# Performance work log

Hardware: AMD Instinct MI355X
Metric: run time of the kernel (lower is better)

Reference implementation:

```python
import jax, jax.numpy as jnp
import numpy as np

N = 100000
E = 1600000
DIMS = [128, 128, 64]


def _gcn_norm(edge_index, num_nodes):
    # PyG gcn_norm: add self-loops, symmetric normalization D^-1/2 (A+I) D^-1/2
    src, dst = edge_index[0], edge_index[1]
    loop = jnp.arange(num_nodes, dtype=src.dtype)
    src = jnp.concatenate([src, loop])
    dst = jnp.concatenate([dst, loop])
    deg = jax.ops.segment_sum(jnp.ones_like(src, dtype=jnp.float32), dst,
                              num_segments=num_nodes)
    dinv = jnp.where(deg > 0, jax.lax.rsqrt(deg), 0.0)
    w = dinv[src] * dinv[dst]  # [E+N]
    return src, dst, w


def _gcn_conv(x, src, dst, w, W, b):
    # transform first (cheaper when out_dim <= in_dim), then aggregate
    h = x @ W                                   # [N, out]
    msg = h[src] * w[:, None]                   # gather + scale  [E+N, out]
    out = jax.ops.segment_sum(msg, dst, num_segments=x.shape[0])
    return out + b


def setup_inputs() -> dict:
    key = jax.random.key(0)
    ks = jax.random.split(key, 6)
    x = jax.random.normal(ks[0], (N, DIMS[0]), dtype=jnp.float32)
    edge_index = jax.random.randint(ks[1], (2, E), 0, N, dtype=jnp.int64)
    # Glorot-style init for GCNConv weights, zero bias (PyG default)
    W1 = jax.random.normal(ks[2], (DIMS[0], DIMS[1]), dtype=jnp.float32) / np.sqrt(DIMS[0])
    b1 = jnp.zeros((DIMS[1],), dtype=jnp.float32)
    W2 = jax.random.normal(ks[3], (DIMS[1], DIMS[2]), dtype=jnp.float32) / np.sqrt(DIMS[1])
    b2 = jnp.zeros((DIMS[2],), dtype=jnp.float32)
    return {"x": x, "edge_index": edge_index, "W1": W1, "b1": b1, "W2": W2, "b2": b2}


def reference(x, edge_index, W1, b1, W2, b2):
    src, dst, w = _gcn_norm(edge_index, x.shape[0])
    h = _gcn_conv(x, src, dst, w, W1, b1)
    h = jax.nn.relu(h)
    # dropout is identity in eval mode (deterministic reference)
    out = _gcn_conv(h, src, dst, w, W2, b2)
    return out
```

## Files before the change

kernel.cpp:

```cpp
#include <hip/hip_runtime.h>
#include <hip/hip_fp16.h>

#define TPB 256
#define CHUNK 1024
#define EPB 4096
#define CSHIFT 8
#define AGG_BLOCKS 2048

typedef _Float16 half8 __attribute__((ext_vector_type(8)));
typedef float    f32x4 __attribute__((ext_vector_type(4)));


__global__ __launch_bounds__(256) void scanA_kernel(const int* __restrict__ cnt,
                                                    int* __restrict__ row_ptr,
                                                    int* __restrict__ chunk_sums, int n) {
    __shared__ int ls[256];
    const int t    = threadIdx.x;
    const int base = blockIdx.x * CHUNK;
    const int idx  = base + t * 4;
    int4 v = make_int4(0, 0, 0, 0);
    if (idx + 3 < n) v = *(const int4*)(cnt + idx);
    else {
        if (idx + 0 < n) v.x = cnt[idx + 0];
        if (idx + 1 < n) v.y = cnt[idx + 1];
        if (idx + 2 < n) v.z = cnt[idx + 2];
        if (idx + 3 < n) v.w = cnt[idx + 3];
    }
    int s0 = v.x, s1 = s0 + v.y, s2 = s1 + v.z, s3 = s2 + v.w;
    ls[t] = s3;
    __syncthreads();
    for (int off = 1; off < 256; off <<= 1) {
        int xv = (t >= off) ? ls[t - off] : 0;
        __syncthreads();
        ls[t] += xv;
        __syncthreads();
    }
    int excl = (t == 0) ? 0 : ls[t - 1];
    if (idx + 0 < n) row_ptr[idx + 0] = excl;
    if (idx + 1 < n) row_ptr[idx + 1] = excl + s0;
    if (idx + 2 < n) row_ptr[idx + 2] = excl + s1;
    if (idx + 3 < n) row_ptr[idx + 3] = excl + s2;
    if (t == 255) chunk_sums[blockIdx.x] = ls[255];
}

__global__ __launch_bounds__(256) void scanB_kernel(int* __restrict__ chunk_sums, int nch) {
    __shared__ int ls[256];
    const int t = threadIdx.x;
    ls[t] = (t < nch) ? chunk_sums[t] : 0;
    __syncthreads();
    for (int off = 1; off < 256; off <<= 1) {
        int xv = (t >= off) ? ls[t - off] : 0;
        __syncthreads();
        ls[t] += xv;
        __syncthreads();
    }
    if (t < nch) chunk_sums[t] = (t == 0) ? 0 : ls[t - 1];
}


__global__ __launch_bounds__(256) void hist_kernel(const int* __restrict__ dst,
                                                   int* __restrict__ hist_g,
                                                   int e, int nbc, int nblk) {
    __shared__ int hs[512];
    const int t = threadIdx.x;
    for (int i = t; i < nbc; i += 256) hs[i] = 0;
    __syncthreads();
    const int e0  = blockIdx.x * EPB;
    const int lim = min(e0 + EPB, e);
    for (int i = e0 + t; i < lim; i += 256)
        atomicAdd(&hs[dst[i] >> CSHIFT], 1);
    __syncthreads();
    for (int b = t; b < nbc; b += 256)
        hist_g[b * nblk + blockIdx.x] = hs[b];
}

__global__ __launch_bounds__(256) void partition_kernel(const int* __restrict__ src,
                                                        const int* __restrict__ dst,
                                                        const int* __restrict__ hist_scan,
                                                        const int* __restrict__ chunk_sums,
                                                        int* __restrict__ pairs,
                                                        int e, int nbc, int nblk) {
    __shared__ int  hs[512];
    __shared__ int  lscan[512];
    __shared__ int  lfill[512];
    __shared__ int  base_s[512];
    __shared__ int  ls[256];
    __shared__ int2 sp[EPB];
    const int t = threadIdx.x;
    for (int i = t; i < nbc; i += 256) { hs[i] = 0; lfill[i] = 0; }
    __syncthreads();
    const int e0  = blockIdx.x * EPB;
    const int lim = min(e0 + EPB, e);
    for (int i = e0 + t; i < lim; i += 256)
        atomicAdd(&hs[dst[i] >> CSHIFT], 1);
    __syncthreads();
    int v0 = (2 * t     < nbc) ? hs[2 * t]     : 0;
    int v1 = (2 * t + 1 < nbc) ? hs[2 * t + 1] : 0;
    ls[t] = v0 + v1;
    __syncthreads();
    for (int off = 1; off < 256; off <<= 1) {
        int xv = (t >= off) ? ls[t - off] : 0;
        __syncthreads();
        ls[t] += xv;
        __syncthreads();
    }
    int excl = (t == 0) ? 0 : ls[t - 1];
    if (2 * t     < nbc) lscan[2 * t]     = excl;
    if (2 * t + 1 < nbc) lscan[2 * t + 1] = excl + v0;
    for (int b = t; b < nbc; b += 256) {
        int hidx = b * nblk + blockIdx.x;
        base_s[b] = hist_scan[hidx] + chunk_sums[hidx >> 10];
    }
    __syncthreads();
    for (int i = e0 + t; i < lim; i += 256) {
        int d = dst[i];
        int b = d >> CSHIFT;
        int r = atomicAdd(&lfill[b], 1);
        sp[lscan[b] + r] = make_int2(src[i], d);
    }
    __syncthreads();
    const int cnt = lim - e0;
    for (int i = t; i < cnt; i += 256) {
        int2 pr = sp[i];
        int  b  = pr.y >> CSHIFT;
        pairs[base_s[b] + (i - lscan[b])] = pr.x | ((pr.y & 255) << 17);
    }
}

__global__ __launch_bounds__(256) void bucket_finalize_kernel(const int* __restrict__ pairs,
                                                              const int* __restrict__ hist_scan,
                                                              const int* __restrict__ chunk_sums,
                                                              int* __restrict__ row_ptr,
                                                              float* __restrict__ dinv,
                                                              int* __restrict__ csr_src,
                                                              int n, int e, int nbc, int nblk) {
    __shared__ int cnt_s[256];
    __shared__ int fill[256];
    __shared__ int ls[256];
    const int b   = blockIdx.x;
    const int nb0 = b << CSHIFT;
    const int t   = threadIdx.x;
    const int h0  = b * nblk;
    const int r0  = hist_scan[h0] + chunk_sums[h0 >> 10];
    int r1 = e;
    if (b + 1 < nbc) {
        const int h1 = (b + 1) * nblk;
        r1 = hist_scan[h1] + chunk_sums[h1 >> 10];
    }
    cnt_s[t] = 0;
    __syncthreads();
    for (int i = r0 + t; i < r1; i += 256)
        atomicAdd(&cnt_s[pairs[i] >> 17], 1);
    __syncthreads();
    int c = cnt_s[t];
    ls[t] = c;
    __syncthreads();
    for (int off = 1; off < 256; off <<= 1) {
        int xv = (t >= off) ? ls[t - off] : 0;
        __syncthreads();
        ls[t] += xv;
        __syncthreads();
    }
    int excl = (t == 0) ? 0 : ls[t - 1];
    int node = nb0 + t;
    if (node < n) {
        row_ptr[node] = r0 + excl;
        dinv[node]    = rsqrtf((float)(c + 1));
    }
    fill[t] = r0 + excl;
    __syncthreads();
    for (int i = r0 + t; i < r1; i += 256) {
        int pr = pairs[i];
        int p  = atomicAdd(&fill[pr >> 17], 1);
        csr_src[p] = pr & 0x1FFFF;
    }
    if (b == 0 && t == 0) row_ptr[n] = e;
}


__global__ __launch_bounds__(256) void wprep_kernel(const float* __restrict__ W1,
                                                    const float* __restrict__ W2,
                                                    _Float16* __restrict__ wf1g,
                                                    _Float16* __restrict__ wf2g) {
    const int tid = threadIdx.x;
    if (blockIdx.x == 0) {
        for (int f = tid; f < 8 * 4 * 64; f += 256) {
            int c    = f >> 8;
            int i    = (f >> 6) & 3;
            int lane = f & 63;
            int quad = lane >> 4, n = lane & 15;
            const float* wp = W1 + (size_t)(i * 32 + quad * 8) * 128 + c * 16 + n;
            half8 hv;
#pragma unroll
            for (int j = 0; j < 8; ++j) hv[j] = (_Float16)wp[(size_t)j * 128];
            ((half8*)wf1g)[f] = hv;
        }
    } else {
        for (int f = tid; f < 4 * 4 * 64; f += 256) {
            int c    = f >> 8;
            int i    = (f >> 6) & 3;
            int lane = f & 63;
            int quad = lane >> 4, n = lane & 15;
            const float* wp = W2 + (size_t)(i * 32 + quad * 8) * 64 + c * 16 + n;
            half8 hv;
#pragma unroll
            for (int j = 0; j < 8; ++j) hv[j] = (_Float16)wp[(size_t)j * 64];
            ((half8*)wf2g)[f] = hv;
        }
    }
}


template <int M, bool RELU, typename XT>
__global__ __launch_bounds__(256) void gemm_mfma_kernel(const XT* __restrict__ X,
                                                        const _Float16* __restrict__ Wfg,
                                                        const float* __restrict__ dinv,
                                                        __half* __restrict__ H, int nrows) {
    constexpr int NC = M / 16;
    __shared__ __align__(16) _Float16 Wf[NC * 4 * 64 * 8];

    const int tid = threadIdx.x;
    const uint4* wb = (const uint4*)Wfg;
    for (int f = tid; f < NC * 4 * 64; f += 256)
        ((uint4*)Wf)[f] = wb[f];
    __syncthreads();

    const int  wave = tid >> 6, lane = tid & 63;
    const int  quad = lane >> 4, n16 = lane & 15;
    const long rowbase = (long)blockIdx.x * 64 + wave * 16;

    long arow = rowbase + n16;
    const XT* xrow = X + (size_t)(arow < nrows ? arow : 0) * 128;
    half8 a[4];
    if constexpr (sizeof(XT) == 4) {
        const float4* xr = (const float4*)xrow;
#pragma unroll
        for (int i = 0; i < 4; ++i) {
            float4 x0 = xr[i * 8 + quad * 2];
            float4 x1 = xr[i * 8 + quad * 2 + 1];
            if (RELU) {
                x0.x = fmaxf(x0.x, 0.f); x0.y = fmaxf(x0.y, 0.f);
                x0.z = fmaxf(x0.z, 0.f); x0.w = fmaxf(x0.w, 0.f);
                x1.x = fmaxf(x1.x, 0.f); x1.y = fmaxf(x1.y, 0.f);
                x1.z = fmaxf(x1.z, 0.f); x1.w = fmaxf(x1.w, 0.f);
            }
            half8 hv;
            hv[0] = (_Float16)x0.x; hv[1] = (_Float16)x0.y;
            hv[2] = (_Float16)x0.z; hv[3] = (_Float16)x0.w;
            hv[4] = (_Float16)x1.x; hv[5] = (_Float16)x1.y;
            hv[6] = (_Float16)x1.z; hv[7] = (_Float16)x1.w;
            a[i] = hv;
        }
    } else {
        const half8* xr = (const half8*)xrow;
#pragma unroll
        for (int i = 0; i < 4; ++i) {
            half8 hv = xr[i * 4 + quad];
            if (RELU) {
#pragma unroll
                for (int j = 0; j < 8; ++j)
                    hv[j] = (hv[j] > (_Float16)0) ? hv[j] : (_Float16)0;
            }
            a[i] = hv;
        }
    }

    float dv[4];
#pragma unroll
    for (int r = 0; r < 4; ++r) {
        long orow = rowbase + quad * 4 + r;
        dv[r] = (orow < nrows) ? dinv[orow] : 0.f;
    }

    for (int c = 0; c < NC; ++c) {
        f32x4 acc = {0.f, 0.f, 0.f, 0.f};
#pragma unroll
        for (int i = 0; i < 4; ++i) {
            half8 b = ((const half8*)Wf)[(c * 4 + i) * 64 + lane];
            acc = __builtin_amdgcn_mfma_f32_16x16x32_f16(a[i], b, acc, 0, 0, 0);
        }
#pragma unroll
        for (int r = 0; r < 4; ++r) {
            long orow = rowbase + quad * 4 + r;
            if (orow < nrows)
                H[orow * M + c * 16 + n16] = __float2half(acc[r] * dv[r]);
        }
    }
}


__device__ __forceinline__ void add_u4(float2* a, const uint4& u) {
    float2 v0 = __half22float2(*(const __half2*)&u.x);
    float2 v1 = __half22float2(*(const __half2*)&u.y);
    float2 v2 = __half22float2(*(const __half2*)&u.z);
    float2 v3 = __half22float2(*(const __half2*)&u.w);
    a[0].x += v0.x; a[0].y += v0.y;
    a[1].x += v1.x; a[1].y += v1.y;
    a[2].x += v2.x; a[2].y += v2.y;
    a[3].x += v3.x; a[3].y += v3.y;
}


__global__ __launch_bounds__(TPB) void agg_pull128_kernel(const __half* __restrict__ hs,
                                                          const int* __restrict__ csr_src,
                                                          const int* __restrict__ row_ptr,
                                                          const float* __restrict__ dinv,
                                                          const float* __restrict__ bias,
                                                          __half* __restrict__ out, int n) {
    const int wid  = blockIdx.x * (TPB / 64) + (threadIdx.x >> 6);
    const int NW   = gridDim.x * (TPB / 64);
    const int lane = threadIdx.x & 63;
    const int q    = lane >> 4;
    const int sl   = lane & 15;
    if (wid >= n) return;
    const uint4* up   = (const uint4*)hs;
    const uint4* upsl = up + sl;

    const float4* bp = (const float4*)bias;
    const float4 bb0 = bp[2 * sl], bb1 = bp[2 * sl + 1];

    int b0 = row_ptr[wid], e0 = row_ptr[wid + 1];
    int nA = wid + NW;
    int b1 = 0, e1 = 0;
    if (nA < n) { b1 = row_ptr[nA]; e1 = row_ptr[nA + 1]; }
    int m0 = e0 - b0; if (m0 > 64) m0 = 64;
    int idx0 = (lane < m0) ? csr_src[b0 + lane] : 0;
    uint4 self0 = make_uint4(0, 0, 0, 0);
    if (q == 0) self0 = up[(size_t)wid * 16 + sl];
    float dv0 = dinv[wid];

    for (int ni = wid; ni < n; ni += NW) {
        const int n1 = ni + NW, n2 = ni + 2 * NW;
        int b2 = 0, e2 = 0;
        if (n2 < n) { b2 = row_ptr[n2]; e2 = row_ptr[n2 + 1]; }
        int idx1 = 0; uint4 self1 = make_uint4(0, 0, 0, 0); float dv1 = 0.f;
        if (n1 < n) {
            int m1 = e1 - b1; if (m1 > 64) m1 = 64;
            idx1 = (lane < m1) ? csr_src[b1 + lane] : 0;
            if (q == 0) self1 = up[(size_t)n1 * 16 + sl];
            dv1 = dinv[n1];
        }
        int m = e0 - b0; if (m > 64) m = 64;
        int sA0 = __shfl(idx0, q);
        int sA1 = __shfl(idx0, 4 + q);
        int sA2 = __shfl(idx0, 8 + q);
        int sA3 = __shfl(idx0, 12 + q);
        int sB0 = __shfl(idx0, 16 + q);
        int sB1 = __shfl(idx0, 20 + q);
        int sB2 = __shfl(idx0, 24 + q);
        int sB3 = __shfl(idx0, 28 + q);
        uint4 uA0 = upsl[(size_t)(unsigned)sA0 * 16];
        uint4 uA1 = upsl[(size_t)(unsigned)sA1 * 16];
        uint4 uA2 = upsl[(size_t)(unsigned)sA2 * 16];
        uint4 uA3 = upsl[(size_t)(unsigned)sA3 * 16];
        uint4 uB0 = upsl[(size_t)(unsigned)sB0 * 16];
        uint4 uB1 = upsl[(size_t)(unsigned)sB1 * 16];
        uint4 uB2 = upsl[(size_t)(unsigned)sB2 * 16];
        uint4 uB3 = upsl[(size_t)(unsigned)sB3 * 16];
        float2 a0[4], a1[4];
#pragma unroll
        for (int k = 0; k < 4; ++k) { a0[k] = make_float2(0.f, 0.f); a1[k] = make_float2(0.f, 0.f); }
        if (m >= 32) {
            add_u4(a0, uA0); add_u4(a1, uA1); add_u4(a0, uA2); add_u4(a1, uA3);
            add_u4(a0, uB0); add_u4(a1, uB1); add_u4(a0, uB2); add_u4(a1, uB3);
        } else {
            if (q < m)      add_u4(a0, uA0);
            if (4 + q < m)  add_u4(a1, uA1);
            if (8 + q < m)  add_u4(a0, uA2);
            if (12 + q < m) add_u4(a1, uA3);
            if (16 + q < m) add_u4(a0, uB0);
            if (20 + q < m) add_u4(a1, uB1);
            if (24 + q < m) add_u4(a0, uB2);
            if (28 + q < m) add_u4(a1, uB3);
        }
        for (int j = 32; j < m; j += 16) {
            int s0 = __shfl(idx0, j + q);
            int s1 = __shfl(idx0, j + 4 + q);
            int s2 = __shfl(idx0, j + 8 + q);
            int s3 = __shfl(idx0, j + 12 + q);
            uint4 u0 = upsl[(size_t)(unsigned)s0 * 16];
            uint4 u1 = upsl[(size_t)(unsigned)s1 * 16];
            uint4 u2 = upsl[(size_t)(unsigned)s2 * 16];
            uint4 u3 = upsl[(size_t)(unsigned)s3 * 16];
            if (j + q < m)      add_u4(a0, u0);
            if (j + 4 + q < m)  add_u4(a1, u1);
            if (j + 8 + q < m)  add_u4(a0, u2);
            if (j + 12 + q < m) add_u4(a1, u3);
        }
        for (int base = b0 + 64; base < e0; base += 64) {
            int mm = e0 - base; if (mm > 64) mm = 64;
            int idxv = (lane < mm) ? csr_src[base + lane] : 0;
            for (int j = 0; j < mm; j += 16) {
                int s0 = __shfl(idxv, j + q);
                int s1 = __shfl(idxv, j + 4 + q);
                int s2 = __shfl(idxv, j + 8 + q);
                int s3 = __shfl(idxv, j + 12 + q);
                uint4 u0 = upsl[(size_t)(unsigned)s0 * 16];
                uint4 u1 = upsl[(size_t)(unsigned)s1 * 16];
                uint4 u2 = upsl[(size_t)(unsigned)s2 * 16];
                uint4 u3 = upsl[(size_t)(unsigned)s3 * 16];
                if (j + q < mm)      add_u4(a0, u0);
                if (j + 4 + q < mm)  add_u4(a1, u1);
                if (j + 8 + q < mm)  add_u4(a0, u2);
                if (j + 12 + q < mm) add_u4(a1, u3);
            }
        }
#pragma unroll
        for (int k = 0; k < 4; ++k) { a0[k].x += a1[k].x; a0[k].y += a1[k].y; }
#pragma unroll
        for (int k = 0; k < 4; ++k) {
            a0[k].x += __shfl(a0[k].x, lane ^ 16);
            a0[k].y += __shfl(a0[k].y, lane ^ 16);
            a0[k].x += __shfl(a0[k].x, lane ^ 32);
            a0[k].y += __shfl(a0[k].y, lane ^ 32);
        }
        if (q == 0) {
            float2 v0 = __half22float2(*(const __half2*)&self0.x);
            float2 v1 = __half22float2(*(const __half2*)&self0.y);
            float2 v2 = __half22float2(*(const __half2*)&self0.z);
            float2 v3 = __half22float2(*(const __half2*)&self0.w);
            __half2 h0 = __floats2half2_rn(bb0.x + dv0 * (a0[0].x + v0.x),
                                           bb0.y + dv0 * (a0[0].y + v0.y));
            __half2 h1 = __floats2half2_rn(bb0.z + dv0 * (a0[1].x + v1.x),
                                           bb0.w + dv0 * (a0[1].y + v1.y));
            __half2 h2 = __floats2half2_rn(bb1.x + dv0 * (a0[2].x + v2.x),
                                           bb1.y + dv0 * (a0[2].y + v2.y));
            __half2 h3 = __floats2half2_rn(bb1.z + dv0 * (a0[3].x + v3.x),
                                           bb1.w + dv0 * (a0[3].y + v3.y));
            uint4 ov;
            ov.x = *(const unsigned*)&h0; ov.y = *(const unsigned*)&h1;
            ov.z = *(const unsigned*)&h2; ov.w = *(const unsigned*)&h3;
            ((uint4*)out)[(size_t)ni * 16 + sl] = ov;
        }
        b0 = b1; e0 = e1; idx0 = idx1; self0 = self1; dv0 = dv1;
        b1 = b2; e1 = e2;
    }
}


__global__ __launch_bounds__(TPB) void agg_pull64_kernel(const __half* __restrict__ hs,
                                                         const int* __restrict__ csr_src,
                                                         const int* __restrict__ row_ptr,
                                                         const float* __restrict__ dinv,
                                                         const float* __restrict__ bias,
                                                         float* __restrict__ out, int n) {
    const int wid  = blockIdx.x * (TPB / 64) + (threadIdx.x >> 6);
    const int NW   = gridDim.x * (TPB / 64);
    const int lane = threadIdx.x & 63;
    const int h    = lane >> 5;
    const int lh   = lane & 31;
    const int qh   = lh >> 3;
    const int sl   = lane & 7;
    const int hb   = h << 5;
    const int npairs = (n + 1) >> 1;
    if (wid >= npairs) return;
    const uint4* up   = (const uint4*)hs;
    const uint4* upsl = up + sl;

    const float4* bp = (const float4*)bias;
    const float4 bb0 = bp[2 * sl], bb1 = bp[2 * sl + 1];

    int np0 = 2 * wid + h;
    int b0 = 0, e0 = 0;
    if (np0 < n) { b0 = row_ptr[np0]; e0 = row_ptr[np0 + 1]; }
    int pA = wid + NW;
    int b1 = 0, e1 = 0;
    {
        int npA = 2 * pA + h;
        if (pA < npairs && npA < n) { b1 = row_ptr[npA]; e1 = row_ptr[npA + 1]; }
    }
    int m0 = e0 - b0; if (m0 > 32) m0 = 32;
    int idx0 = (lh < m0) ? csr_src[b0 + lh] : 0;
    uint4 self0 = make_uint4(0, 0, 0, 0);
    if (qh == 0 && np0 < n) self0 = up[(size_t)np0 * 8 + sl];
    float dv0 = (np0 < n) ? dinv[np0] : 0.f;

    for (int pp = wid; pp < npairs; pp += NW) {
        const int p1 = pp + NW, p2 = pp + 2 * NW;
        const int np = 2 * pp + h;
        int b2 = 0, e2 = 0;
        if (p2 < npairs) {
            int np2 = 2 * p2 + h;
            if (np2 < n) { b2 = row_ptr[np2]; e2 = row_ptr[np2 + 1]; }
        }
        int idx1 = 0; uint4 self1 = make_uint4(0, 0, 0, 0); float dv1 = 0.f;
        if (p1 < npairs) {
            int np1 = 2 * p1 + h;
            if (np1 < n) {
                int m1 = e1 - b1; if (m1 > 32) m1 = 32;
                idx1 = (lh < m1) ? csr_src[b1 + lh] : 0;
                if (qh == 0) self1 = up[(size_t)np1 * 8 + sl];
                dv1 = dinv[np1];
            }
        }
        int m = e0 - b0; if (m > 32) m = 32;
        int s0 = __shfl(idx0, hb + qh);
        int s1 = __shfl(idx0, hb + 4 + qh);
        int s2 = __shfl(idx0, hb + 8 + qh);
        int s3 = __shfl(idx0, hb + 12 + qh);
        int s4 = __shfl(idx0, hb + 16 + qh);
        int s5 = __shfl(idx0, hb + 20 + qh);
        int s6 = __shfl(idx0, hb + 24 + qh);
        int s7 = __shfl(idx0, hb + 28 + qh);
        uint4 u0 = upsl[(size_t)(unsigned)s0 * 8];
        uint4 u1 = upsl[(size_t)(unsigned)s1 * 8];
        uint4 u2 = upsl[(size_t)(unsigned)s2 * 8];
        uint4 u3 = upsl[(size_t)(unsigned)s3 * 8];
        uint4 u4 = upsl[(size_t)(unsigned)s4 * 8];
        uint4 u5 = upsl[(size_t)(unsigned)s5 * 8];
        uint4 u6 = upsl[(size_t)(unsigned)s6 * 8];
        uint4 u7 = upsl[(size_t)(unsigned)s7 * 8];
        float2 a0[4], a1[4];
#pragma unroll
        for (int k = 0; k < 4; ++k) { a0[k] = make_float2(0.f, 0.f); a1[k] = make_float2(0.f, 0.f); }
        if (m >= 32) {
            add_u4(a0, u0); add_u4(a1, u1); add_u4(a0, u2); add_u4(a1, u3);
            add_u4(a0, u4); add_u4(a1, u5); add_u4(a0, u6); add_u4(a1, u7);
        } else {
            if (qh < m)      add_u4(a0, u0);
            if (4 + qh < m)  add_u4(a1, u1);
            if (8 + qh < m)  add_u4(a0, u2);
            if (12 + qh < m) add_u4(a1, u3);
            if (16 + qh < m) add_u4(a0, u4);
            if (20 + qh < m) add_u4(a1, u5);
            if (24 + qh < m) add_u4(a0, u6);
            if (28 + qh < m) add_u4(a1, u7);
        }
        for (int base = b0 + 32; base < e0; base += 32) {
            int mm = e0 - base; if (mm > 32) mm = 32;
            int idxv = (lh < mm) ? csr_src[base + lh] : 0;
            for (int j = 0; j < mm; j += 8) {
                int t0 = __shfl(idxv, hb + j + qh);
                int t1 = __shfl(idxv, hb + j + 4 + qh);
                uint4 v0 = upsl[(size_t)(unsigned)t0 * 8];
                uint4 v1 = upsl[(size_t)(unsigned)t1 * 8];
                if (j + qh < mm)     add_u4(a0, v0);
                if (j + 4 + qh < mm) add_u4(a1, v1);
            }
        }
#pragma unroll
        for (int k = 0; k < 4; ++k) { a0[k].x += a1[k].x; a0[k].y += a1[k].y; }
#pragma unroll
        for (int k = 0; k < 4; ++k) {
            a0[k].x += __shfl(a0[k].x, lane ^ 8);
            a0[k].y += __shfl(a0[k].y, lane ^ 8);
            a0[k].x += __shfl(a0[k].x, lane ^ 16);
            a0[k].y += __shfl(a0[k].y, lane ^ 16);
        }
        if (qh == 0 && np < n) {
            float2 v0 = __half22float2(*(const __half2*)&self0.x);
            float2 v1 = __half22float2(*(const __half2*)&self0.y);
            float2 v2 = __half22float2(*(const __half2*)&self0.z);
            float2 v3 = __half22float2(*(const __half2*)&self0.w);
            float4 o0, o1;
            o0.x = bb0.x + dv0 * (a0[0].x + v0.x);
            o0.y = bb0.y + dv0 * (a0[0].y + v0.y);
            o0.z = bb0.z + dv0 * (a0[1].x + v1.x);
            o0.w = bb0.w + dv0 * (a0[1].y + v1.y);
            o1.x = bb1.x + dv0 * (a0[2].x + v2.x);
            o1.y = bb1.y + dv0 * (a0[2].y + v2.y);
            o1.z = bb1.z + dv0 * (a0[3].x + v3.x);
            o1.w = bb1.w + dv0 * (a0[3].y + v3.y);
            ((float4*)out)[(size_t)np * 16 + 2 * sl]     = o0;
            ((float4*)out)[(size_t)np * 16 + 2 * sl + 1] = o1;
        }
        b0 = b1; e0 = e1; idx0 = idx1; self0 = self1; dv0 = dv1;
        b1 = b2; e1 = e2;
    }
}


extern "C" void kernel_launch(void* const* d_in, const int* in_sizes, int n_in,
                              void* d_out, int out_size, void* d_ws, size_t ws_size,
                              hipStream_t stream) {
    const float* x  = (const float*)d_in[0];
    const int*   ei = (const int*)d_in[1];
    const float* W1 = (const float*)d_in[2];
    const float* b1 = (const float*)d_in[3];
    const float* W2 = (const float*)d_in[4];
    const float* b2 = (const float*)d_in[5];
    float* out = (float*)d_out;

    const int N = in_sizes[0] / 128;
    const int E = in_sizes[1] / 2;
    const int* srcv = ei;
    const int* dstv = ei + E;

    const int NBC    = (N + 255) >> CSHIFT;
    const int NBLK_E = (E + EPB - 1) / EPB;
    const int HLEN   = NBC * NBLK_E;
    const int NCHH   = (HLEN + CHUNK - 1) / CHUNK;

    char* p = (char*)d_ws;
    int*      row_ptr    = (int*)p;      p += (((size_t)N + 64) * 4 + 63) & ~(size_t)63;
    int*      chunk_sums = (int*)p;      p += 1024;
    int*      hist       = (int*)p;      p += (((size_t)HLEN + 64) * 4 + 63) & ~(size_t)63;
    int*      csr_src    = (int*)p;      p += ((size_t)E * 4 + 63) & ~(size_t)63;
    float*    dinv       = (float*)p;    p += (((size_t)N + 64) * 4 + 63) & ~(size_t)63;
    _Float16* wf1g       = (_Float16*)p; p += 8 * 4 * 64 * 16;
    _Float16* wf2g       = (_Float16*)p; p += 4 * 4 * 64 * 16;
    __half*   hs1        = (__half*)p;   p += (size_t)N * 128 * 2;
    __half*   out1       = (__half*)p;   p += (size_t)N * 128 * 2;
    int*      pairs      = (int*)out1;
    __half*   hs2        = hs1;

    wprep_kernel<<<2, 256, 0, stream>>>(W1, W2, wf1g, wf2g);

    hist_kernel<<<NBLK_E, 256, 0, stream>>>(dstv, hist, E, NBC, NBLK_E);
    scanA_kernel<<<NCHH, 256, 0, stream>>>(hist, hist, chunk_sums, HLEN);
    scanB_kernel<<<1, 256, 0, stream>>>(chunk_sums, NCHH);
    partition_kernel<<<NBLK_E, 256, 0, stream>>>(srcv, dstv, hist, chunk_sums, pairs,
                                                 E, NBC, NBLK_E);
    bucket_finalize_kernel<<<NBC, 256, 0, stream>>>(pairs, hist, chunk_sums, row_ptr, dinv,
                                                    csr_src, N, E, NBC, NBLK_E);

    gemm_mfma_kernel<128, false, float><<<(N + 63) / 64, 256, 0, stream>>>(x, wf1g, dinv, hs1, N);
    agg_pull128_kernel<<<AGG_BLOCKS, TPB, 0, stream>>>(hs1, csr_src, row_ptr, dinv, b1, out1, N);

    gemm_mfma_kernel<64, true, _Float16><<<(N + 63) / 64, 256, 0, stream>>>(
        (const _Float16*)out1, wf2g, dinv, hs2, N);
    agg_pull64_kernel<<<AGG_BLOCKS, TPB, 0, stream>>>(hs2, csr_src, row_ptr, dinv, b2, out, N);
}
```

Baseline: 259.8 us.

## Replace bucketed partition CSR build with global-atomic degree count and placement

Replaces the two-level bucket-sort CSR construction (histogram, partition through shared memory, per-bucket finalize) with a plain counting sort. Global atomics count per-node degree, a scan builds row_ptr, and a second pass of global atomics places each source into csr_src. Weight preparation is folded into the degree kernel to save a launch. The new path uses fewer kernels and passes over the data, but the global atomics are scattered, and the order of neighbours within a row becomes nondeterministic, which hurts locality in the gather.

```diff
diff --git a/kernel.cpp b/kernel.cpp
--- a/kernel.cpp
+++ b/kernel.cpp
@@ -3,12 +3,52 @@
 
 #define TPB 256
 #define CHUNK 1024
-#define EPB 4096
-#define CSHIFT 8
 #define AGG_BLOCKS 2048
 
 typedef _Float16 half8 __attribute__((ext_vector_type(8)));
 typedef float    f32x4 __attribute__((ext_vector_type(4)));
+
+
+__global__ __launch_bounds__(256) void deg_wprep_kernel(const int* __restrict__ dst,
+                                                        int* __restrict__ deg,
+                                                        const float* __restrict__ W1,
+                                                        const float* __restrict__ W2,
+                                                        _Float16* __restrict__ wf1g,
+                                                        _Float16* __restrict__ wf2g,
+                                                        int e) {
+    const int t = threadIdx.x;
+    if (blockIdx.x == 0) {
+        for (int f = t; f < 8 * 4 * 64; f += 256) {
+            int c = f >> 8, i = (f >> 6) & 3, lane = f & 63;
+            int quad = lane >> 4, nn = lane & 15;
+            const float* wp = W1 + (size_t)(i * 32 + quad * 8) * 128 + c * 16 + nn;
+            half8 hv;
+#pragma unroll
+            for (int j = 0; j < 8; ++j) hv[j] = (_Float16)wp[(size_t)j * 128];
+            ((half8*)wf1g)[f] = hv;
+        }
+    } else if (blockIdx.x == 1) {
+        for (int f = t; f < 4 * 4 * 64; f += 256) {
+            int c = f >> 8, i = (f >> 6) & 3, lane = f & 63;
+            int quad = lane >> 4, nn = lane & 15;
+            const float* wp = W2 + (size_t)(i * 32 + quad * 8) * 64 + c * 16 + nn;
+            half8 hv;
+#pragma unroll
+            for (int j = 0; j < 8; ++j) hv[j] = (_Float16)wp[(size_t)j * 64];
+            ((half8*)wf2g)[f] = hv;
+        }
+    }
+    const int idx = (blockIdx.x * 256 + t) * 4;
+    if (idx + 3 < e) {
+        int4 d = *(const int4*)(dst + idx);
+        atomicAdd(&deg[d.x], 1);
+        atomicAdd(&deg[d.y], 1);
+        atomicAdd(&deg[d.z], 1);
+        atomicAdd(&deg[d.w], 1);
+    } else {
+        for (int i = idx; i < e; ++i) atomicAdd(&deg[dst[i]], 1);
+    }
+}
 
 
 __global__ __launch_bounds__(256) void scanA_kernel(const int* __restrict__ cnt,
@@ -58,154 +98,56 @@
 }
 
 
-__global__ __launch_bounds__(256) void hist_kernel(const int* __restrict__ dst,
-                                                   int* __restrict__ hist_g,
-                                                   int e, int nbc, int nblk) {
-    __shared__ int hs[512];
-    const int t = threadIdx.x;
-    for (int i = t; i < nbc; i += 256) hs[i] = 0;
-    __syncthreads();
-    const int e0  = blockIdx.x * EPB;
-    const int lim = min(e0 + EPB, e);
-    for (int i = e0 + t; i < lim; i += 256)
-        atomicAdd(&hs[dst[i] >> CSHIFT], 1);
-    __syncthreads();
-    for (int b = t; b < nbc; b += 256)
-        hist_g[b * nblk + blockIdx.x] = hs[b];
-}
-
-__global__ __launch_bounds__(256) void partition_kernel(const int* __restrict__ src,
-                                                        const int* __restrict__ dst,
-                                                        const int* __restrict__ hist_scan,
-                                                        const int* __restrict__ chunk_sums,
-                                                        int* __restrict__ pairs,
-                                                        int e, int nbc, int nblk) {
-    __shared__ int  hs[512];
-    __shared__ int  lscan[512];
-    __shared__ int  lfill[512];
-    __shared__ int  base_s[512];
-    __shared__ int  ls[256];
-    __shared__ int2 sp[EPB];
-    const int t = threadIdx.x;
-    for (int i = t; i < nbc; i += 256) { hs[i] = 0; lfill[i] = 0; }
-    __syncthreads();
-    const int e0  = blockIdx.x * EPB;
-    const int lim = min(e0 + EPB, e);
-    for (int i = e0 + t; i < lim; i += 256)
-        atomicAdd(&hs[dst[i] >> CSHIFT], 1);
-    __syncthreads();
-    int v0 = (2 * t     < nbc) ? hs[2 * t]     : 0;
-    int v1 = (2 * t + 1 < nbc) ? hs[2 * t + 1] : 0;
-    ls[t] = v0 + v1;
-    __syncthreads();
-    for (int off = 1; off < 256; off <<= 1) {
-        int xv = (t >= off) ? ls[t - off] : 0;
-        __syncthreads();
-        ls[t] += xv;
-        __syncthreads();
-    }
-    int excl = (t == 0) ? 0 : ls[t - 1];
-    if (2 * t     < nbc) lscan[2 * t]     = excl;
-    if (2 * t + 1 < nbc) lscan[2 * t + 1] = excl + v0;
-    for (int b = t; b < nbc; b += 256) {
-        int hidx = b * nblk + blockIdx.x;
-        base_s[b] = hist_scan[hidx] + chunk_sums[hidx >> 10];
-    }
-    __syncthreads();
-    for (int i = e0 + t; i < lim; i += 256) {
-        int d = dst[i];
-        int b = d >> CSHIFT;
-        int r = atomicAdd(&lfill[b], 1);
-        sp[lscan[b] + r] = make_int2(src[i], d);
-    }
-    __syncthreads();
-    const int cnt = lim - e0;
-    for (int i = t; i < cnt; i += 256) {
-        int2 pr = sp[i];
-        int  b  = pr.y >> CSHIFT;
-        pairs[base_s[b] + (i - lscan[b])] = pr.x | ((pr.y & 255) << 17);
-    }
-}
-
-__global__ __launch_bounds__(256) void bucket_finalize_kernel(const int* __restrict__ pairs,
-                                                              const int* __restrict__ hist_scan,
-                                                              const int* __restrict__ chunk_sums,
-                                                              int* __restrict__ row_ptr,
-                                                              float* __restrict__ dinv,
-                                                              int* __restrict__ csr_src,
-                                                              int n, int e, int nbc, int nblk) {
-    __shared__ int cnt_s[256];
-    __shared__ int fill[256];
-    __shared__ int ls[256];
-    const int b   = blockIdx.x;
-    const int nb0 = b << CSHIFT;
-    const int t   = threadIdx.x;
-    const int h0  = b * nblk;
-    const int r0  = hist_scan[h0] + chunk_sums[h0 >> 10];
-    int r1 = e;
-    if (b + 1 < nbc) {
-        const int h1 = (b + 1) * nblk;
-        r1 = hist_scan[h1] + chunk_sums[h1 >> 10];
-    }
-    cnt_s[t] = 0;
-    __syncthreads();
-    for (int i = r0 + t; i < r1; i += 256)
-        atomicAdd(&cnt_s[pairs[i] >> 17], 1);
-    __syncthreads();
-    int c = cnt_s[t];
-    ls[t] = c;
-    __syncthreads();
-    for (int off = 1; off < 256; off <<= 1) {
-        int xv = (t >= off) ? ls[t - off] : 0;
-        __syncthreads();
-        ls[t] += xv;
-        __syncthreads();
-    }
-    int excl = (t == 0) ? 0 : ls[t - 1];
-    int node = nb0 + t;
-    if (node < n) {
-        row_ptr[node] = r0 + excl;
-        dinv[node]    = rsqrtf((float)(c + 1));
-    }
-    fill[t] = r0 + excl;
-    __syncthreads();
-    for (int i = r0 + t; i < r1; i += 256) {
-        int pr = pairs[i];
-        int p  = atomicAdd(&fill[pr >> 17], 1);
-        csr_src[p] = pr & 0x1FFFF;
-    }
-    if (b == 0 && t == 0) row_ptr[n] = e;
-}
-
-
-__global__ __launch_bounds__(256) void wprep_kernel(const float* __restrict__ W1,
-                                                    const float* __restrict__ W2,
-                                                    _Float16* __restrict__ wf1g,
-                                                    _Float16* __restrict__ wf2g) {
-    const int tid = threadIdx.x;
-    if (blockIdx.x == 0) {
-        for (int f = tid; f < 8 * 4 * 64; f += 256) {
-            int c    = f >> 8;
-            int i    = (f >> 6) & 3;
-            int lane = f & 63;
-            int quad = lane >> 4, n = lane & 15;
-            const float* wp = W1 + (size_t)(i * 32 + quad * 8) * 128 + c * 16 + n;
-            half8 hv;
-#pragma unroll
-            for (int j = 0; j < 8; ++j) hv[j] = (_Float16)wp[(size_t)j * 128];
-            ((half8*)wf1g)[f] = hv;
-        }
+__global__ __launch_bounds__(256) void fixup_kernel(int* __restrict__ row_ptr,
+                                                    int* __restrict__ fill,
+                                                    const int* __restrict__ deg,
+                                                    float* __restrict__ dinv,
+                                                    const int* __restrict__ chunk_sums,
+                                                    int n, int e) {
+    const int t    = threadIdx.x;
+    const int base = blockIdx.x * CHUNK;
+    const int off  = chunk_sums[blockIdx.x];
+    const int idx  = base + t * 4;
+    if (idx + 3 < n) {
+        int4 rp = *(const int4*)(row_ptr + idx);
+        int4 dg = *(const int4*)(deg + idx);
+        rp.x += off; rp.y += off; rp.z += off; rp.w += off;
+        *(int4*)(row_ptr + idx) = rp;
+        *(int4*)(fill + idx)    = rp;
+        float4 dv;
+        dv.x = rsqrtf((float)(dg.x + 1));
+        dv.y = rsqrtf((float)(dg.y + 1));
+        dv.z = rsqrtf((float)(dg.z + 1));
+        dv.w = rsqrtf((float)(dg.w + 1));
+        *(float4*)(dinv + idx) = dv;
     } else {
-        for (int f = tid; f < 4 * 4 * 64; f += 256) {
-            int c    = f >> 8;
-            int i    = (f >> 6) & 3;
-            int lane = f & 63;
-            int quad = lane >> 4, n = lane & 15;
-            const float* wp = W2 + (size_t)(i * 32 + quad * 8) * 64 + c * 16 + n;
-            half8 hv;
-#pragma unroll
-            for (int j = 0; j < 8; ++j) hv[j] = (_Float16)wp[(size_t)j * 64];
-            ((half8*)wf2g)[f] = hv;
+        for (int i = idx; i < n; ++i) {
+            int rp = row_ptr[i] + off;
+            row_ptr[i] = rp;
+            fill[i]    = rp;
+            dinv[i]    = rsqrtf((float)(deg[i] + 1));
+        }
+    }
+    if (blockIdx.x == 0 && t == 0) row_ptr[n] = e;
+}
+
+
+__global__ __launch_bounds__(256) void place_kernel(const int* __restrict__ src,
+                                                    const int* __restrict__ dst,
+                                                    int* __restrict__ fill,
+                                                    int* __restrict__ csr_src, int e) {
+    const int idx = (blockIdx.x * 256 + threadIdx.x) * 4;
+    if (idx + 3 < e) {
+        int4 d = *(const int4*)(dst + idx);
+        int4 s = *(const int4*)(src + idx);
+        int p0 = atomicAdd(&fill[d.x], 1); csr_src[p0] = s.x;
+        int p1 = atomicAdd(&fill[d.y], 1); csr_src[p1] = s.y;
+        int p2 = atomicAdd(&fill[d.z], 1); csr_src[p2] = s.z;
+        int p3 = atomicAdd(&fill[d.w], 1); csr_src[p3] = s.w;
+    } else {
+        for (int i = idx; i < e; ++i) {
+            int p = atomicAdd(&fill[dst[i]], 1);
+            csr_src[p] = src[i];
         }
     }
 }
@@ -586,33 +528,29 @@
     const int* srcv = ei;
     const int* dstv = ei + E;
 
-    const int NBC    = (N + 255) >> CSHIFT;
-    const int NBLK_E = (E + EPB - 1) / EPB;
-    const int HLEN   = NBC * NBLK_E;
-    const int NCHH   = (HLEN + CHUNK - 1) / CHUNK;
+    const int NCH_N  = (N + CHUNK - 1) / CHUNK;
+    const int EBLK   = (E + 1023) / 1024;
 
     char* p = (char*)d_ws;
     int*      row_ptr    = (int*)p;      p += (((size_t)N + 64) * 4 + 63) & ~(size_t)63;
+    int*      deg        = (int*)p;      p += (((size_t)N + 64) * 4 + 63) & ~(size_t)63;
+    int*      fill       = (int*)p;      p += (((size_t)N + 64) * 4 + 63) & ~(size_t)63;
     int*      chunk_sums = (int*)p;      p += 1024;
-    int*      hist       = (int*)p;      p += (((size_t)HLEN + 64) * 4 + 63) & ~(size_t)63;
     int*      csr_src    = (int*)p;      p += ((size_t)E * 4 + 63) & ~(size_t)63;
     float*    dinv       = (float*)p;    p += (((size_t)N + 64) * 4 + 63) & ~(size_t)63;
     _Float16* wf1g       = (_Float16*)p; p += 8 * 4 * 64 * 16;
     _Float16* wf2g       = (_Float16*)p; p += 4 * 4 * 64 * 16;
     __half*   hs1        = (__half*)p;   p += (size_t)N * 128 * 2;
     __half*   out1       = (__half*)p;   p += (size_t)N * 128 * 2;
-    int*      pairs      = (int*)out1;
     __half*   hs2        = hs1;
 
-    wprep_kernel<<<2, 256, 0, stream>>>(W1, W2, wf1g, wf2g);
-
-    hist_kernel<<<NBLK_E, 256, 0, stream>>>(dstv, hist, E, NBC, NBLK_E);
-    scanA_kernel<<<NCHH, 256, 0, stream>>>(hist, hist, chunk_sums, HLEN);
-    scanB_kernel<<<1, 256, 0, stream>>>(chunk_sums, NCHH);
-    partition_kernel<<<NBLK_E, 256, 0, stream>>>(srcv, dstv, hist, chunk_sums, pairs,
-                                                 E, NBC, NBLK_E);
-    bucket_finalize_kernel<<<NBC, 256, 0, stream>>>(pairs, hist, chunk_sums, row_ptr, dinv,
-                                                    csr_src, N, E, NBC, NBLK_E);
+    hipMemsetAsync(deg, 0, (size_t)N * 4, stream);
+
+    deg_wprep_kernel<<<EBLK, 256, 0, stream>>>(dstv, deg, W1, W2, wf1g, wf2g, E);
+    scanA_kernel<<<NCH_N, 256, 0, stream>>>(deg, row_ptr, chunk_sums, N);
+    scanB_kernel<<<1, 256, 0, stream>>>(chunk_sums, NCH_N);
+    fixup_kernel<<<NCH_N, 256, 0, stream>>>(row_ptr, fill, deg, dinv, chunk_sums, N, E);
+    place_kernel<<<EBLK, 256, 0, stream>>>(srcv, dstv, fill, csr_src, E);
 
     gemm_mfma_kernel<128, false, float><<<(N + 63) / 64, 256, 0, stream>>>(x, wf1g, dinv, hs1, N);
     agg_pull128_kernel<<<AGG_BLOCKS, TPB, 0, stream>>>(hs1, csr_src, row_ptr, dinv, b1, out1, N);
```

Result: slower. 402.1 us (+54.8%).
